# Kernel optimization log

Hardware: AMD Instinct MI355X
Metric: run time of the kernel (lower is better)

The kernel has to match this reference:

```python
import jax, jax.numpy as jnp
import numpy as np

B, N, H = 8, 256, 128


def _linear_params(key, fin, fout):
    # torch nn.Linear default init: U(-1/sqrt(fin), 1/sqrt(fin)) for weight and bias
    k1, k2 = jax.random.split(key)
    lim = 1.0 / np.sqrt(fin)
    w = jax.random.uniform(k1, (fin, fout), jnp.float32, -lim, lim)
    b = jax.random.uniform(k2, (fout,), jnp.float32, -lim, lim)
    return w, b


def setup_inputs() -> dict:
    key = jax.random.key(0)
    ks = jax.random.split(key, 12)
    inp = {
        'x': jax.random.normal(ks[0], (B, N, 3), jnp.float32),
        'h': jax.random.normal(ks[1], (B, N, H), jnp.float32),
        'x0': jax.random.normal(ks[2], (B, N, 3), jnp.float32),
        'pad_mask': jnp.ones((B, N, 1), jnp.float32),
    }
    names_dims = [
        ('edg1', 2 * H + 2, H), ('edg2', H, H), ('edgi', H, 1),
        ('node1', 2 * H, H), ('node2', H, H),
        ('cor1', 2 * H + 2, H), ('cor2', H, H), ('cor3', H, 1),
    ]
    for i, (name, fin, fout) in enumerate(names_dims):
        w, b = _linear_params(ks[3 + i], fin, fout)
        inp[name + '_w'] = w
        inp[name + '_b'] = b
    return inp


def _safe_dist(d2):
    # sqrt with zero (not NaN) gradient where d2 == 0 (diagonal)
    pos = d2 > 0
    return jnp.sqrt(jnp.where(pos, d2, 1.0)) * pos


def reference(x, h, x0, pad_mask,
              edg1_w, edg1_b, edg2_w, edg2_b, edgi_w, edgi_b,
              node1_w, node1_b, node2_w, node2_b,
              cor1_w, cor1_b, cor2_w, cor2_b, cor3_w, cor3_b):
    silu = jax.nn.silu
    b, n, hd = h.shape
    # pairwise squared distances, shapes (b, n, n, 1)
    diff0 = x0[:, :, None, :] - x0[:, None, :, :]
    d0_2 = jnp.sum(diff0 * diff0, axis=-1, keepdims=True)
    diff = x[:, :, None, :] - x[:, None, :, :]
    d2 = jnp.sum(diff * diff, axis=-1, keepdims=True)
    dist = _safe_dist(d2)
    # all-pairs node-feature concat: pair[b,i,j] = [h_i, h_j, d2_ij, d0_2_ij]
    hi = jnp.broadcast_to(h[:, :, None, :], (b, n, n, hd))
    hj = jnp.broadcast_to(h[:, None, :, :], (b, n, n, hd))
    pair = jnp.concatenate([hi, hj, d2, d0_2], axis=-1)  # (b,n,n,2H+2)
    # edge MLP -> messages
    m = silu(silu(pair @ edg1_w + edg1_b) @ edg2_w + edg2_b)  # (b,n,n,H)
    e = jax.nn.sigmoid(m @ edgi_w + edgi_b)                   # (b,n,n,1)
    offdiag = 1.0 - jnp.eye(n, dtype=x.dtype)[None, :, :, None]
    e = e * offdiag
    agg = jnp.mean(e * m, axis=2)  # mean over j -> (b,n,H)
    # node update with residual
    nin = jnp.concatenate([h, agg], axis=-1)
    h_next = h + (silu(nin @ node1_w + node1_b) @ node2_w + node2_b)
    # coordinate update
    cw = silu(silu(pair @ cor1_w + cor1_b) @ cor2_w + cor2_b) @ cor3_w + cor3_b  # (b,n,n,1)
    shift = diff / (dist + 1.0)
    upd = jnp.mean(cw * shift * offdiag, axis=2)  # (b,n,3)
    x_next = x + upd
    if pad_mask is not None:
        x_next = x_next * pad_mask
        h_next = h_next * pad_mask
    return x_next, h_next
```

## Files before the change

### kernel.cpp

```cpp
#include <hip/hip_runtime.h>

typedef __attribute__((ext_vector_type(8))) short short8;
typedef __attribute__((ext_vector_type(8))) unsigned short ushort8_t;
typedef __attribute__((ext_vector_type(4))) float f32x4;

#define BN 256
#define HD 128
#define WSTRIDE 136

__device__ __forceinline__ unsigned short f2bf(float f) {
    union { float f; unsigned int i; } v; v.f = f;
    unsigned int lsb = (v.i >> 16) & 1u;
    v.i += 0x7fffu + lsb;
    return (unsigned short)(v.i >> 16);
}
__device__ __forceinline__ float fsigmoid(float x) {
    return __builtin_amdgcn_rcpf(1.0f + __expf(-x));
}
__device__ __forceinline__ float fsilu(float x) {
    return x * fsigmoid(x);
}

__global__ __launch_bounds__(256) void prep_w(const float* __restrict__ e2w,
                                              const float* __restrict__ c2w,
                                              unsigned short* __restrict__ WtE,
                                              unsigned short* __restrict__ WtC) {
    int n = blockIdx.x;
    int t = threadIdx.x;
    if (t < 128) WtE[n * 128 + t] = f2bf(e2w[t * 128 + n]);
    else         WtC[n * 128 + (t - 128)] = f2bf(c2w[(t - 128) * 128 + n]);
}

__global__ __launch_bounds__(256) void prep_A(const float* __restrict__ h,
                                              const float* __restrict__ e1w,
                                              const float* __restrict__ e1b,
                                              const float* __restrict__ c1w,
                                              const float* __restrict__ c1b,
                                              float* __restrict__ A1e, float* __restrict__ A2e,
                                              float* __restrict__ A1c, float* __restrict__ A2c) {
    int r0 = blockIdx.x * 4;
    int k   = threadIdx.x & 127;
    int grp = threadIdx.x >> 7;
    __shared__ float hsl[4][HD];
    {
        int rr = threadIdx.x >> 7;
        hsl[rr][k]     = h[(r0 + rr) * HD + k];
        hsl[rr + 2][k] = h[(r0 + rr + 2) * HD + k];
    }
    __syncthreads();
    const float* W = grp ? c1w : e1w;
    float s1[4] = {0,0,0,0}, s2[4] = {0,0,0,0};
#pragma unroll 4
    for (int f = 0; f < HD; ++f) {
        float w1 = W[f * HD + k];
        float w2 = W[(HD + f) * HD + k];
#pragma unroll
        for (int r = 0; r < 4; ++r) {
            float hv = hsl[r][f];
            s1[r] += hv * w1; s2[r] += hv * w2;
        }
    }
    float bb = grp ? c1b[k] : e1b[k];
    float* O1 = grp ? A1c : A1e;
    float* O2 = grp ? A2c : A2e;
#pragma unroll
    for (int r = 0; r < 4; ++r) {
        O1[(r0 + r) * HD + k] = s1[r] + bb;
        O2[(r0 + r) * HD + k] = s2[r];
    }
}

__global__ __launch_bounds__(1024, 4) void egc_main(
    const float* __restrict__ x, const float* __restrict__ h,
    const float* __restrict__ x0, const float* __restrict__ pmask,
    const float* __restrict__ e1w,
    const float* __restrict__ e2b, const float* __restrict__ eiw,
    const float* __restrict__ eib,
    const float* __restrict__ n1w, const float* __restrict__ n1b,
    const float* __restrict__ n2w, const float* __restrict__ n2b,
    const float* __restrict__ c1w, const float* __restrict__ c2b,
    const float* __restrict__ c3w, const float* __restrict__ c3b,
    const float* __restrict__ A1e, const float* __restrict__ A2e,
    const float* __restrict__ A1c, const float* __restrict__ A2c,
    const unsigned short* __restrict__ WtE, const unsigned short* __restrict__ WtC,
    float* __restrict__ xout, float* __restrict__ hout) {

    __shared__ __align__(16) unsigned short WtEl[HD * WSTRIDE];
    __shared__ __align__(16) unsigned short WtCl[HD * WSTRIDE];
    __shared__ __align__(16) float xs[BN][4];
    __shared__ __align__(16) float x0s[BN][4];
    __shared__ __align__(16) float d2s[BN], d02s[BN], rsh[BN];
    __shared__ __align__(16) float vE0[HD], vE1[HD], vE2[HD];
    __shared__ __align__(16) float vC0[HD], vC1[HD], vC2[HD];
    __shared__ __align__(16) float hsv[HD];
    __shared__ __align__(16) float aggbuf[16][HD];
    __shared__ __align__(16) float aggv[HD];
    __shared__ float updbuf[16][4];
    __shared__ float smask;

    const int tid = threadIdx.x;
    const int bi  = blockIdx.x;
    const int b   = bi >> 8;
    const int i   = bi & 255;
    const int row = bi;

#pragma unroll
    for (int u = 0; u < 2; ++u) {
        int idx = u * 1024 + tid;
        int n   = idx >> 4;
        int k8  = (idx & 15) * 8;
        *(ushort8_t*)(WtEl + n * WSTRIDE + k8) = *(const ushort8_t*)(WtE + n * HD + k8);
        *(ushort8_t*)(WtCl + n * WSTRIDE + k8) = *(const ushort8_t*)(WtC + n * HD + k8);
    }

    if (tid < BN) {
        int gj = b * BN + tid;
        xs[tid][0]  = x[gj * 3 + 0];
        xs[tid][1]  = x[gj * 3 + 1];
        xs[tid][2]  = x[gj * 3 + 2];
        x0s[tid][0] = x0[gj * 3 + 0];
        x0s[tid][1] = x0[gj * 3 + 1];
        x0s[tid][2] = x0[gj * 3 + 2];
    } else if (tid < BN + HD) {
        int t = tid - BN;
        vE0[t] = A1e[row * HD + t];
        vE1[t] = e1w[256 * HD + t];
        vE2[t] = e1w[257 * HD + t];
    } else if (tid < BN + 2 * HD) {
        int t = tid - BN - HD;
        vC0[t] = A1c[row * HD + t];
        vC1[t] = c1w[256 * HD + t];
        vC2[t] = c1w[257 * HD + t];
    } else if (tid < BN + 3 * HD) {
        int t = tid - BN - 2 * HD;
        hsv[t] = h[row * HD + t];
    }
    if (tid == 1023) smask = pmask[row];
    __syncthreads();

    if (tid < BN) {
        float dx = xs[i][0] - xs[tid][0];
        float dy = xs[i][1] - xs[tid][1];
        float dz = xs[i][2] - xs[tid][2];
        float d2 = dx * dx + dy * dy + dz * dz;
        d2s[tid] = d2;
        float dist = (d2 > 0.0f) ? sqrtf(d2) : 0.0f;
        rsh[tid] = __builtin_amdgcn_rcpf(dist + 1.0f);
        float ex = x0s[i][0] - x0s[tid][0];
        float ey = x0s[i][1] - x0s[tid][1];
        float ez = x0s[i][2] - x0s[tid][2];
        d02s[tid] = ex * ex + ey * ey + ez * ez;
    }
    __syncthreads();

    const int lane = tid & 63, wv = tid >> 6;
    const int c = lane & 15, q = lane >> 4;
    const int ra = wv * 16 + c;

    {
        const float* A2g = A2e + (size_t)b * BN * HD;
        f32x4 acc[8];
        const f32x4 zf = {0.f, 0.f, 0.f, 0.f};
#pragma unroll
        for (int nt = 0; nt < 8; ++nt) acc[nt] = zf;
        const float d2v = d2s[ra], d02v = d02s[ra];
#pragma unroll
        for (int ks = 0; ks < 4; ++ks) {
            const int kb = ks * 32 + q * 8;
            float4 alo = *(const float4*)(A2g + ra * HD + kb);
            float4 ahi = *(const float4*)(A2g + ra * HD + kb + 4);
            float4 p0 = *(const float4*)(vE0 + kb);
            float4 p0h = *(const float4*)(vE0 + kb + 4);
            float4 p1 = *(const float4*)(vE1 + kb);
            float4 p1h = *(const float4*)(vE1 + kb + 4);
            float4 p2 = *(const float4*)(vE2 + kb);
            float4 p2h = *(const float4*)(vE2 + kb + 4);
            short8 af;
            af[0] = (short)f2bf(fsilu(alo.x + p0.x + d2v * p1.x + d02v * p2.x));
            af[1] = (short)f2bf(fsilu(alo.y + p0.y + d2v * p1.y + d02v * p2.y));
            af[2] = (short)f2bf(fsilu(alo.z + p0.z + d2v * p1.z + d02v * p2.z));
            af[3] = (short)f2bf(fsilu(alo.w + p0.w + d2v * p1.w + d02v * p2.w));
            af[4] = (short)f2bf(fsilu(ahi.x + p0h.x + d2v * p1h.x + d02v * p2h.x));
            af[5] = (short)f2bf(fsilu(ahi.y + p0h.y + d2v * p1h.y + d02v * p2h.y));
            af[6] = (short)f2bf(fsilu(ahi.z + p0h.z + d2v * p1h.z + d02v * p2h.z));
            af[7] = (short)f2bf(fsilu(ahi.w + p0h.w + d2v * p1h.w + d02v * p2h.w));
#pragma unroll
            for (int nt = 0; nt < 8; ++nt) {
                short8 Bf = *(const short8*)(WtEl + (nt * 16 + c) * WSTRIDE + kb);
                acc[nt] = __builtin_amdgcn_mfma_f32_16x16x32_bf16(af, Bf, acc[nt], 0, 0, 0);
            }
        }
        float b2l[8], wIl[8];
#pragma unroll
        for (int nt = 0; nt < 8; ++nt) {
            b2l[nt] = e2b[nt * 16 + c];
            wIl[nt] = eiw[nt * 16 + c];
        }
        float bI = eib[0];
        float aggp[8] = {0,0,0,0,0,0,0,0};
#pragma unroll
        for (int reg = 0; reg < 4; ++reg) {
            int r = wv * 16 + q * 4 + reg;
            float mv[8]; float ed = 0.f;
#pragma unroll
            for (int nt = 0; nt < 8; ++nt) {
                mv[nt] = fsilu(acc[nt][reg] + b2l[nt]);
                ed += mv[nt] * wIl[nt];
            }
            ed += __shfl_xor(ed, 1);
            ed += __shfl_xor(ed, 2);
            ed += __shfl_xor(ed, 4);
            ed += __shfl_xor(ed, 8);
            float e = (r == i) ? 0.0f : fsigmoid(ed + bI);
#pragma unroll
            for (int nt = 0; nt < 8; ++nt) aggp[nt] += e * mv[nt];
        }
#pragma unroll
        for (int nt = 0; nt < 8; ++nt) {
            aggp[nt] += __shfl_xor(aggp[nt], 16);
            aggp[nt] += __shfl_xor(aggp[nt], 32);
        }
        if (q == 0)
#pragma unroll
            for (int nt = 0; nt < 8; ++nt) aggbuf[wv][nt * 16 + c] = aggp[nt];
    }
    __syncthreads();
    if (tid < HD) {
        float s = 0.f;
#pragma unroll
        for (int w = 0; w < 16; ++w) s += aggbuf[w][tid];
        aggv[tid] = s * (1.0f / 256.0f);
    }
    __syncthreads();

    {
        const float* A2g = A2c + (size_t)b * BN * HD;
        f32x4 acc[8];
        const f32x4 zf = {0.f, 0.f, 0.f, 0.f};
#pragma unroll
        for (int nt = 0; nt < 8; ++nt) acc[nt] = zf;
        const float d2v = d2s[ra], d02v = d02s[ra];
#pragma unroll
        for (int ks = 0; ks < 4; ++ks) {
            const int kb = ks * 32 + q * 8;
            float4 alo = *(const float4*)(A2g + ra * HD + kb);
            float4 ahi = *(const float4*)(A2g + ra * HD + kb + 4);
            float4 p0 = *(const float4*)(vC0 + kb);
            float4 p0h = *(const float4*)(vC0 + kb + 4);
            float4 p1 = *(const float4*)(vC1 + kb);
            float4 p1h = *(const float4*)(vC1 + kb + 4);
            float4 p2 = *(const float4*)(vC2 + kb);
            float4 p2h = *(const float4*)(vC2 + kb + 4);
            short8 af;
            af[0] = (short)f2bf(fsilu(alo.x + p0.x + d2v * p1.x + d02v * p2.x));
            af[1] = (short)f2bf(fsilu(alo.y + p0.y + d2v * p1.y + d02v * p2.y));
            af[2] = (short)f2bf(fsilu(alo.z + p0.z + d2v * p1.z + d02v * p2.z));
            af[3] = (short)f2bf(fsilu(alo.w + p0.w + d2v * p1.w + d02v * p2.w));
            af[4] = (short)f2bf(fsilu(ahi.x + p0h.x + d2v * p1h.x + d02v * p2h.x));
            af[5] = (short)f2bf(fsilu(ahi.y + p0h.y + d2v * p1h.y + d02v * p2h.y));
            af[6] = (short)f2bf(fsilu(ahi.z + p0h.z + d2v * p1h.z + d02v * p2h.z));
            af[7] = (short)f2bf(fsilu(ahi.w + p0h.w + d2v * p1h.w + d02v * p2h.w));
#pragma unroll
            for (int nt = 0; nt < 8; ++nt) {
                short8 Bf = *(const short8*)(WtCl + (nt * 16 + c) * WSTRIDE + kb);
                acc[nt] = __builtin_amdgcn_mfma_f32_16x16x32_bf16(af, Bf, acc[nt], 0, 0, 0);
            }
        }
        float b2l[8], w3l[8];
#pragma unroll
        for (int nt = 0; nt < 8; ++nt) {
            b2l[nt] = c2b[nt * 16 + c];
            w3l[nt] = c3w[nt * 16 + c];
        }
        float b3 = c3b[0];
        float updp = 0.f;
        float xic = (c < 3) ? xs[i][c] : 0.f;
#pragma unroll
        for (int reg = 0; reg < 4; ++reg) {
            int r = wv * 16 + q * 4 + reg;
            float cd = 0.f;
#pragma unroll
            for (int nt = 0; nt < 8; ++nt)
                cd += fsilu(acc[nt][reg] + b2l[nt]) * w3l[nt];
            cd += __shfl_xor(cd, 1);
            cd += __shfl_xor(cd, 2);
            cd += __shfl_xor(cd, 4);
            cd += __shfl_xor(cd, 8);
            float cw = cd + b3;
            if (c < 3 && r != i)
                updp += cw * (xic - xs[r][c]) * rsh[r];
        }
        updp += __shfl_xor(updp, 16);
        updp += __shfl_xor(updp, 32);
        if (q == 0 && c < 3) updbuf[wv][c] = updp;
    }
    __syncthreads();

    if (tid < 3) {
        float u = 0.f;
#pragma unroll
        for (int w = 0; w < 16; ++w) u += updbuf[w][tid];
        u *= (1.0f / 256.0f);
        xout[row * 3 + tid] = (xs[i][tid] + u) * smask;
    }

    float* npart = &aggbuf[0][0];
    float* qv    = &aggbuf[8][0];
    {
        int k = tid & 127, part = tid >> 7;
        const float* src = (part < 4) ? hsv : aggv;
        int fbase = (part & 3) * 32;
        int wrow = ((part < 4) ? 0 : HD) + fbase;
        float s = 0.f;
#pragma unroll 4
        for (int f = 0; f < 32; ++f)
            s += src[fbase + f] * n1w[(size_t)(wrow + f) * HD + k];
        npart[part * HD + k] = s;
    }
    __syncthreads();
    if (tid < HD) {
        float s = n1b[tid];
#pragma unroll
        for (int p = 0; p < 8; ++p) s += npart[p * HD + tid];
        qv[tid] = fsilu(s);
    }
    __syncthreads();
    {
        int o = tid & 127, p = tid >> 7;
        float s = 0.f;
#pragma unroll 4
        for (int f = 0; f < 16; ++f) {
            int ff = p * 16 + f;
            s += qv[ff] * n2w[(size_t)ff * HD + o];
        }
        npart[p * HD + o] = s;
    }
    __syncthreads();
    if (tid < HD) {
        float s = 0.f;
#pragma unroll
        for (int p = 0; p < 8; ++p) s += npart[p * HD + tid];
        hout[(size_t)row * HD + tid] = (hsv[tid] + s + n2b[tid]) * smask;
    }
}

extern "C" void kernel_launch(void* const* d_in, const int* in_sizes, int n_in,
                              void* d_out, int out_size, void* d_ws, size_t ws_size,
                              hipStream_t stream) {
    const float* x    = (const float*)d_in[0];
    const float* h    = (const float*)d_in[1];
    const float* x0   = (const float*)d_in[2];
    const float* pm   = (const float*)d_in[3];
    const float* e1w  = (const float*)d_in[4];
    const float* e1b  = (const float*)d_in[5];
    const float* e2w  = (const float*)d_in[6];
    const float* e2b  = (const float*)d_in[7];
    const float* eiw  = (const float*)d_in[8];
    const float* eib  = (const float*)d_in[9];
    const float* n1w  = (const float*)d_in[10];
    const float* n1b  = (const float*)d_in[11];
    const float* n2w  = (const float*)d_in[12];
    const float* n2b  = (const float*)d_in[13];
    const float* c1w  = (const float*)d_in[14];
    const float* c1b  = (const float*)d_in[15];
    const float* c2w  = (const float*)d_in[16];
    const float* c2b  = (const float*)d_in[17];
    const float* c3w  = (const float*)d_in[18];
    const float* c3b  = (const float*)d_in[19];

    float* wsf = (float*)d_ws;
    const size_t nA = 2048 * 128;
    float* A1e = wsf;
    float* A2e = wsf + nA;
    float* A1c = wsf + 2 * nA;
    float* A2c = wsf + 3 * nA;
    unsigned short* WtE = (unsigned short*)(wsf + 4 * nA);
    unsigned short* WtC = WtE + 128 * 128;

    float* xout = (float*)d_out;
    float* hout = xout + 8 * 256 * 3;

    prep_w<<<dim3(128), dim3(256), 0, stream>>>(e2w, c2w, WtE, WtC);
    prep_A<<<dim3(512), dim3(256), 0, stream>>>(h, e1w, e1b, c1w, c1b, A1e, A2e, A1c, A2c);
    egc_main<<<dim3(2048), dim3(1024), 0, stream>>>(
        x, h, x0, pm, e1w, e2b, eiw, eib, n1w, n1b, n2w, n2b,
        c1w, c2b, c3w, c3b, A1e, A2e, A1c, A2c, WtE, WtC, xout, hout);
}
```

Baseline: 253.4 us.

## Share one LDS weight buffer in main kernel and move prep GEMM to MFMA

The main kernel now keeps a single LDS buffer for the second-layer weights. It loads the edge weights first and reloads the coordinate weights after the aggregation barrier, roughly halving the LDS footprint. The launch-bounds occupancy hint rises from 4 to 8 to match. The node-feature projection prep kernel is rewritten as a bf16 MFMA GEMM over pre-transposed bf16 first-layer weights, replacing the scalar fp32 loop. This adds a second global-to-LDS weight load per block and lowers the precision of the per-node projections.

```diff
diff --git a/kernel.cpp b/kernel.cpp
--- a/kernel.cpp
+++ b/kernel.cpp
@@ -21,56 +21,78 @@
     return x * fsigmoid(x);
 }
 
-__global__ __launch_bounds__(256) void prep_w(const float* __restrict__ e2w,
-                                              const float* __restrict__ c2w,
-                                              unsigned short* __restrict__ WtE,
-                                              unsigned short* __restrict__ WtC) {
-    int n = blockIdx.x;
+__global__ __launch_bounds__(256) void prep_tw(const float* __restrict__ e2w,
+                                               const float* __restrict__ c2w,
+                                               const float* __restrict__ e1w,
+                                               const float* __restrict__ c1w,
+                                               unsigned short* __restrict__ WtE,
+                                               unsigned short* __restrict__ WtC,
+                                               unsigned short* __restrict__ W1e1,
+                                               unsigned short* __restrict__ W1e2,
+                                               unsigned short* __restrict__ W1c1,
+                                               unsigned short* __restrict__ W1c2) {
+    int k = blockIdx.x;
     int t = threadIdx.x;
-    if (t < 128) WtE[n * 128 + t] = f2bf(e2w[t * 128 + n]);
-    else         WtC[n * 128 + (t - 128)] = f2bf(c2w[(t - 128) * 128 + n]);
-}
-
-__global__ __launch_bounds__(256) void prep_A(const float* __restrict__ h,
-                                              const float* __restrict__ e1w,
-                                              const float* __restrict__ e1b,
-                                              const float* __restrict__ c1w,
-                                              const float* __restrict__ c1b,
-                                              float* __restrict__ A1e, float* __restrict__ A2e,
-                                              float* __restrict__ A1c, float* __restrict__ A2c) {
-    int r0 = blockIdx.x * 4;
-    int k   = threadIdx.x & 127;
-    int grp = threadIdx.x >> 7;
-    __shared__ float hsl[4][HD];
-    {
-        int rr = threadIdx.x >> 7;
-        hsl[rr][k]     = h[(r0 + rr) * HD + k];
-        hsl[rr + 2][k] = h[(r0 + rr + 2) * HD + k];
-    }
-    __syncthreads();
-    const float* W = grp ? c1w : e1w;
-    float s1[4] = {0,0,0,0}, s2[4] = {0,0,0,0};
-#pragma unroll 4
-    for (int f = 0; f < HD; ++f) {
-        float w1 = W[f * HD + k];
-        float w2 = W[(HD + f) * HD + k];
-#pragma unroll
-        for (int r = 0; r < 4; ++r) {
-            float hv = hsl[r][f];
-            s1[r] += hv * w1; s2[r] += hv * w2;
-        }
-    }
-    float bb = grp ? c1b[k] : e1b[k];
-    float* O1 = grp ? A1c : A1e;
-    float* O2 = grp ? A2c : A2e;
-#pragma unroll
-    for (int r = 0; r < 4; ++r) {
-        O1[(r0 + r) * HD + k] = s1[r] + bb;
-        O2[(r0 + r) * HD + k] = s2[r];
-    }
-}
-
-__global__ __launch_bounds__(1024, 4) void egc_main(
+    int n = t & 127;
+    if (t < 128) {
+        WtE [n * 128 + k] = f2bf(e2w[k * 128 + n]);
+        W1e1[n * 128 + k] = f2bf(e1w[k * 128 + n]);
+        W1e2[n * 128 + k] = f2bf(e1w[(128 + k) * 128 + n]);
+    } else {
+        WtC [n * 128 + k] = f2bf(c2w[k * 128 + n]);
+        W1c1[n * 128 + k] = f2bf(c1w[k * 128 + n]);
+        W1c2[n * 128 + k] = f2bf(c1w[(128 + k) * 128 + n]);
+    }
+}
+
+__global__ __launch_bounds__(256) void prep_gemm(
+    const float* __restrict__ h,
+    const unsigned short* __restrict__ W1e1, const unsigned short* __restrict__ W1e2,
+    const unsigned short* __restrict__ W1c1, const unsigned short* __restrict__ W1c2,
+    const float* __restrict__ e1b, const float* __restrict__ c1b,
+    float* __restrict__ A1e, float* __restrict__ A2e,
+    float* __restrict__ A1c, float* __restrict__ A2c) {
+    const int tid = threadIdx.x;
+    const int lane = tid & 63, wv = tid >> 6;
+    const int c = lane & 15, q = lane >> 4;
+    const int r0 = blockIdx.x * 16;
+
+    const unsigned short* Wt = (wv == 0) ? W1e1 : (wv == 1) ? W1e2 : (wv == 2) ? W1c1 : W1c2;
+    float* O = (wv == 0) ? A1e : (wv == 1) ? A2e : (wv == 2) ? A1c : A2c;
+    const float* bias = (wv == 0) ? e1b : (wv == 2) ? c1b : (const float*)0;
+
+    f32x4 acc[8];
+    const f32x4 zf = {0.f, 0.f, 0.f, 0.f};
+#pragma unroll
+    for (int nt = 0; nt < 8; ++nt) acc[nt] = zf;
+
+    const float* hrow = h + (size_t)(r0 + c) * HD;
+#pragma unroll
+    for (int ks = 0; ks < 4; ++ks) {
+        const int kb = ks * 32 + q * 8;
+        float4 hlo = *(const float4*)(hrow + kb);
+        float4 hhi = *(const float4*)(hrow + kb + 4);
+        short8 af;
+        af[0] = (short)f2bf(hlo.x); af[1] = (short)f2bf(hlo.y);
+        af[2] = (short)f2bf(hlo.z); af[3] = (short)f2bf(hlo.w);
+        af[4] = (short)f2bf(hhi.x); af[5] = (short)f2bf(hhi.y);
+        af[6] = (short)f2bf(hhi.z); af[7] = (short)f2bf(hhi.w);
+#pragma unroll
+        for (int nt = 0; nt < 8; ++nt) {
+            short8 Bf = *(const short8*)(Wt + (nt * 16 + c) * HD + kb);
+            acc[nt] = __builtin_amdgcn_mfma_f32_16x16x32_bf16(af, Bf, acc[nt], 0, 0, 0);
+        }
+    }
+#pragma unroll
+    for (int nt = 0; nt < 8; ++nt) {
+        float bb = bias ? bias[nt * 16 + c] : 0.f;
+#pragma unroll
+        for (int reg = 0; reg < 4; ++reg)
+            O[(size_t)(r0 + q * 4 + reg) * HD + nt * 16 + c] = acc[nt][reg] + bb;
+    }
+}
+
+__global__ __launch_bounds__(1024, 8) void egc_main(
     const float* __restrict__ x, const float* __restrict__ h,
     const float* __restrict__ x0, const float* __restrict__ pmask,
     const float* __restrict__ e1w,
@@ -85,8 +107,7 @@
     const unsigned short* __restrict__ WtE, const unsigned short* __restrict__ WtC,
     float* __restrict__ xout, float* __restrict__ hout) {
 
-    __shared__ __align__(16) unsigned short WtEl[HD * WSTRIDE];
-    __shared__ __align__(16) unsigned short WtCl[HD * WSTRIDE];
+    __shared__ __align__(16) unsigned short Wl[HD * WSTRIDE];
     __shared__ __align__(16) float xs[BN][4];
     __shared__ __align__(16) float x0s[BN][4];
     __shared__ __align__(16) float d2s[BN], d02s[BN], rsh[BN];
@@ -109,8 +130,7 @@
         int idx = u * 1024 + tid;
         int n   = idx >> 4;
         int k8  = (idx & 15) * 8;
-        *(ushort8_t*)(WtEl + n * WSTRIDE + k8) = *(const ushort8_t*)(WtE + n * HD + k8);
-        *(ushort8_t*)(WtCl + n * WSTRIDE + k8) = *(const ushort8_t*)(WtC + n * HD + k8);
+        *(ushort8_t*)(Wl + n * WSTRIDE + k8) = *(const ushort8_t*)(WtE + n * HD + k8);
     }
 
     if (tid < BN) {
@@ -186,7 +206,7 @@
             af[7] = (short)f2bf(fsilu(ahi.w + p0h.w + d2v * p1h.w + d02v * p2h.w));
 #pragma unroll
             for (int nt = 0; nt < 8; ++nt) {
-                short8 Bf = *(const short8*)(WtEl + (nt * 16 + c) * WSTRIDE + kb);
+                short8 Bf = *(const short8*)(Wl + (nt * 16 + c) * WSTRIDE + kb);
                 acc[nt] = __builtin_amdgcn_mfma_f32_16x16x32_bf16(af, Bf, acc[nt], 0, 0, 0);
             }
         }
@@ -225,11 +245,19 @@
             for (int nt = 0; nt < 8; ++nt) aggbuf[wv][nt * 16 + c] = aggp[nt];
     }
     __syncthreads();
+
     if (tid < HD) {
         float s = 0.f;
 #pragma unroll
         for (int w = 0; w < 16; ++w) s += aggbuf[w][tid];
         aggv[tid] = s * (1.0f / 256.0f);
+    }
+#pragma unroll
+    for (int u = 0; u < 2; ++u) {
+        int idx = u * 1024 + tid;
+        int n   = idx >> 4;
+        int k8  = (idx & 15) * 8;
+        *(ushort8_t*)(Wl + n * WSTRIDE + k8) = *(const ushort8_t*)(WtC + n * HD + k8);
     }
     __syncthreads();
 
@@ -262,7 +290,7 @@
             af[7] = (short)f2bf(fsilu(ahi.w + p0h.w + d2v * p1h.w + d02v * p2h.w));
 #pragma unroll
             for (int nt = 0; nt < 8; ++nt) {
-                short8 Bf = *(const short8*)(WtCl + (nt * 16 + c) * WSTRIDE + kb);
+                short8 Bf = *(const short8*)(Wl + (nt * 16 + c) * WSTRIDE + kb);
                 acc[nt] = __builtin_amdgcn_mfma_f32_16x16x32_bf16(af, Bf, acc[nt], 0, 0, 0);
             }
         }
@@ -374,14 +402,20 @@
     float* A2e = wsf + nA;
     float* A1c = wsf + 2 * nA;
     float* A2c = wsf + 3 * nA;
-    unsigned short* WtE = (unsigned short*)(wsf + 4 * nA);
-    unsigned short* WtC = WtE + 128 * 128;
+    unsigned short* WtE  = (unsigned short*)(wsf + 4 * nA);
+    unsigned short* WtC  = WtE  + 128 * 128;
+    unsigned short* W1e1 = WtC  + 128 * 128;
+    unsigned short* W1e2 = W1e1 + 128 * 128;
+    unsigned short* W1c1 = W1e2 + 128 * 128;
+    unsigned short* W1c2 = W1c1 + 128 * 128;
 
     float* xout = (float*)d_out;
     float* hout = xout + 8 * 256 * 3;
 
-    prep_w<<<dim3(128), dim3(256), 0, stream>>>(e2w, c2w, WtE, WtC);
-    prep_A<<<dim3(512), dim3(256), 0, stream>>>(h, e1w, e1b, c1w, c1b, A1e, A2e, A1c, A2c);
+    prep_tw<<<dim3(128), dim3(256), 0, stream>>>(e2w, c2w, e1w, c1w,
+                                                 WtE, WtC, W1e1, W1e2, W1c1, W1c2);
+    prep_gemm<<<dim3(128), dim3(256), 0, stream>>>(h, W1e1, W1e2, W1c1, W1c2,
+                                                   e1b, c1b, A1e, A2e, A1c, A2c);
     egc_main<<<dim3(2048), dim3(1024), 0, stream>>>(
         x, h, x0, pm, e1w, e2b, eiw, eib, n1w, n1b, n2w, n2b,
         c1w, c2b, c3w, c3b, A1e, A2e, A1c, A2c, WtE, WtC, xout, hout);
```

Measured after the change: 221.9 us. 1.14x faster.
